# Kernel optimization log

Measured on AMD Instinct MI355X. Metric: run time of the kernel, lower is better.

The kernel has to match this reference:

```python
import jax, jax.numpy as jnp
import numpy as np

NUM_EXPERTS = 64
TOP_K = 6
ALPHA = 1e-3
HIDDEN = 128


def setup_inputs() -> dict:
    key = jax.random.key(0)
    k1, k2 = jax.random.split(key)
    hidden_states = jax.random.normal(k1, (64, 4096, HIDDEN), dtype=jnp.float32)
    # kaiming_uniform_(a=sqrt(5)) on weight of shape (64, 128): bound = 1/sqrt(fan_in)
    bound = 1.0 / np.sqrt(HIDDEN)
    W = jax.random.uniform(k2, (NUM_EXPERTS, HIDDEN), dtype=jnp.float32, minval=-bound, maxval=bound)
    return {"hidden_states": hidden_states, "W": W}


def reference(hidden_states, W):
    b, s, h = hidden_states.shape
    x = hidden_states.reshape(-1, h)                      # (N, h)
    logits = x @ W.T                                      # (N, 64)
    scores = jax.nn.softmax(logits, axis=-1)
    topk_weight, topk_idx = jax.lax.top_k(scores, TOP_K)  # (N, 6)
    # norm_topk_prob=True
    topk_weight = topk_weight / (topk_weight.sum(-1, keepdims=True) + 1e-20)
    # aux loss (training path, seq_aux=False): ce = one_hot(topk_idx).mean(0)
    counts = jnp.zeros(NUM_EXPERTS, dtype=scores.dtype).at[topk_idx.ravel()].add(1.0)
    ce = counts / jnp.asarray(topk_idx.size, scores.dtype)
    Pi = scores.mean(0)
    fi = ce * NUM_EXPERTS
    aux_loss = (Pi * fi).sum() * ALPHA
    return topk_idx, topk_weight, aux_loss
```

## Files before the change

### kernel.cpp

```cpp
#include <hip/hip_runtime.h>
#include <cfloat>

#define NTOK (64 * 4096)
#define HID  128
#define NE   64
#define TK   6
#define BLK  256
#define GRID (NTOK / BLK)

__global__ __launch_bounds__(BLK, 4)
void gate_kernel(const float* __restrict__ X,
                 const float* __restrict__ W,
                 float* __restrict__ oidx,
                 float* __restrict__ ow,
                 float* __restrict__ Pi_g,
                 unsigned int* __restrict__ cnt_g)
{
    __shared__ float        Wt[HID][NE];
    __shared__ float        Pi_s[NE];
    __shared__ unsigned int cnt_s[NE];

    const int tid  = threadIdx.x;
    const int lane = tid & 63;

    if (tid < NE) { Pi_s[tid] = 0.0f; cnt_s[tid] = 0u; }

    {
        const float4* W4 = (const float4*)W;
#pragma unroll
        for (int i = 0; i < 8; ++i) {
            const int flat = tid + i * BLK;
            const float4 v = W4[flat];
            const int e   = flat >> 5;
            const int k0  = (flat & 31) << 2;
            const int col = (e + ((flat & 15) << 2)) & 63;
            Wt[k0+0][col] = v.x; Wt[k0+1][col] = v.y;
            Wt[k0+2][col] = v.z; Wt[k0+3][col] = v.w;
        }
    }
    __syncthreads();

    const int token = blockIdx.x * BLK + tid;
    const float4* xrow = (const float4*)(X + (size_t)token * HID);

    float acc[NE];
#pragma unroll
    for (int e = 0; e < NE; ++e) acc[e] = 0.0f;

#pragma unroll 1
    for (int c = 0; c < 8; ++c) {
        float x[16];
#pragma unroll
        for (int j = 0; j < 4; ++j) {
            const float4 v = xrow[c*4 + j];
            x[4*j+0] = v.x; x[4*j+1] = v.y; x[4*j+2] = v.z; x[4*j+3] = v.w;
        }
#pragma unroll
        for (int kk = 0; kk < 16; ++kk) {
            const int row  = c*16 + kk;
            const int rot4 = (row >> 2) & 15;
            const float4* wrow = (const float4*)&Wt[row][0];
#pragma unroll
            for (int q = 0; q < 16; ++q) {
                const float4 w = wrow[(q + rot4) & 15];
                acc[4*q+0] = fmaf(x[kk], w.x, acc[4*q+0]);
                acc[4*q+1] = fmaf(x[kk], w.y, acc[4*q+1]);
                acc[4*q+2] = fmaf(x[kk], w.z, acc[4*q+2]);
                acc[4*q+3] = fmaf(x[kk], w.w, acc[4*q+3]);
            }
        }
    }

    float tv[TK];
    int   ti[TK];
#pragma unroll
    for (int q = 0; q < TK; ++q) { tv[q] = -FLT_MAX; ti[q] = 0; }

#pragma unroll
    for (int e = 0; e < NE; ++e) {
        float m = acc[e];
        int   mi = e;
#pragma unroll
        for (int q = 0; q < TK; ++q) {
            const bool  c  = m > tv[q];
            const float nt = c ? m     : tv[q];
            const float nm = c ? tv[q] : m;
            const int   ni = c ? mi    : ti[q];
            const int   nj = c ? ti[q] : mi;
            tv[q] = nt; m = nm; ti[q] = ni; mi = nj;
        }
    }

    const float mx = tv[0];
    float ex[TK];
    float s = 0.0f;
#pragma unroll
    for (int q = 0; q < TK; ++q) { ex[q] = __expf(tv[q] - mx); s += ex[q]; }
    const float rs = 1.0f / (s + 1e-20f);

    {
        const size_t gt = (size_t)token * TK;
        float2* ip = (float2*)(oidx + gt);
        float2* wp = (float2*)(ow + gt);
        ip[0] = make_float2((float)ti[0], (float)ti[1]);
        ip[1] = make_float2((float)ti[2], (float)ti[3]);
        ip[2] = make_float2((float)ti[4], (float)ti[5]);
        wp[0] = make_float2(ex[0]*rs, ex[1]*rs);
        wp[1] = make_float2(ex[2]*rs, ex[3]*rs);
        wp[2] = make_float2(ex[4]*rs, ex[5]*rs);
    }

#pragma unroll
    for (int q = 0; q < TK; ++q) atomicAdd(&cnt_s[ti[q]], 1u);

    float Z = 0.0f;
#pragma unroll
    for (int e = 0; e < NE; ++e) { acc[e] = __expf(acc[e] - mx); Z += acc[e]; }
    const float rz = 1.0f / Z;
#pragma unroll
    for (int e = 0; e < NE; ++e) acc[e] *= rz;

#pragma unroll
    for (int s = 32; s >= 1; s >>= 1) {
        const bool up = (lane & s) != 0;
#pragma unroll
        for (int i = 0; i < s; ++i) {
            const float lo = acc[i], hi = acc[i + s];
            const float send = up ? lo : hi;
            const float recv = __shfl_xor(send, s);
            acc[i] = (up ? hi : lo) + recv;
        }
    }
    atomicAdd(&Pi_s[lane], acc[0]);

    __syncthreads();
    if (tid < NE) {
        atomicAdd(&Pi_g[tid], Pi_s[tid]);
        atomicAdd(&cnt_g[tid], cnt_s[tid]);
    }
}

__global__ void aux_kernel(const float* __restrict__ Pi_g,
                           const unsigned int* __restrict__ cnt_g,
                           float* __restrict__ out_aux)
{
    const int e = threadIdx.x;
    const float Pi = Pi_g[e] * (1.0f / (float)NTOK);
    const float ce = (float)cnt_g[e] * (1.0f / (float)(NTOK * TK));
    float v = Pi * ce * (float)NE;
#pragma unroll
    for (int off = 32; off > 0; off >>= 1) v += __shfl_down(v, off);
    if (e == 0) out_aux[0] = v * 1.0e-3f;
}

extern "C" void kernel_launch(void* const* d_in, const int* in_sizes, int n_in,
                              void* d_out, int out_size, void* d_ws, size_t ws_size,
                              hipStream_t stream) {
    const float* X = (const float*)d_in[0];
    const float* W = (const float*)d_in[1];

    float* out  = (float*)d_out;
    float* oidx = out;
    float* ow   = out + (size_t)NTOK * TK;
    float* aux  = out + (size_t)NTOK * TK * 2;

    float*        Pi_g  = (float*)d_ws;
    unsigned int* cnt_g = (unsigned int*)((char*)d_ws + 256);

    hipMemsetAsync(d_ws, 0, 512, stream);
    gate_kernel<<<GRID, BLK, 0, stream>>>(X, W, oidx, ow, Pi_g, cnt_g);
    aux_kernel<<<1, 64, 0, stream>>>(Pi_g, cnt_g, aux);
}
```

Before: 258.0 us.

## Register-tile gate GEMM as 4 tokens x 8 experts per thread with staged X chunks

```diff
diff --git a/kernel.cpp b/kernel.cpp
--- a/kernel.cpp
+++ b/kernel.cpp
@@ -6,9 +6,14 @@
 #define NE   64
 #define TK   6
 #define BLK  256
-#define GRID (NTOK / BLK)
-
-__global__ __launch_bounds__(BLK, 4)
+#define TPB  128
+#define GRID (NTOK / TPB)
+#define WST  68
+#define XOFF (HID * WST)
+#define KC   16
+#define NCH  (HID / KC)
+
+__global__ __launch_bounds__(BLK, 3)
 void gate_kernel(const float* __restrict__ X,
                  const float* __restrict__ W,
                  float* __restrict__ oidx,
@@ -16,12 +21,18 @@
                  float* __restrict__ Pi_g,
                  unsigned int* __restrict__ cnt_g)
 {
-    __shared__ float        Wt[HID][NE];
+    __shared__ float smem[XOFF + TPB * KC];
     __shared__ float        Pi_s[NE];
     __shared__ unsigned int cnt_s[NE];
 
     const int tid  = threadIdx.x;
     const int lane = tid & 63;
+    const int wv   = tid >> 6;
+    const int tg   = lane >> 3;
+    const int eg   = lane & 7;
+    const int sw   = tg & 3;
+    const int tokL0 = wv * 32 + tg * 4;
+    const int gtok0 = blockIdx.x * TPB;
 
     if (tid < NE) { Pi_s[tid] = 0.0f; cnt_s[tid] = 0u; }
 
@@ -31,75 +42,107 @@
         for (int i = 0; i < 8; ++i) {
             const int flat = tid + i * BLK;
             const float4 v = W4[flat];
-            const int e   = flat >> 5;
-            const int k0  = (flat & 31) << 2;
-            const int col = (e + ((flat & 15) << 2)) & 63;
-            Wt[k0+0][col] = v.x; Wt[k0+1][col] = v.y;
-            Wt[k0+2][col] = v.z; Wt[k0+3][col] = v.w;
-        }
-    }
-    __syncthreads();
-
-    const int token = blockIdx.x * BLK + tid;
-    const float4* xrow = (const float4*)(X + (size_t)token * HID);
-
-    float acc[NE];
-#pragma unroll
-    for (int e = 0; e < NE; ++e) acc[e] = 0.0f;
+            const int e = flat >> 5, k4 = flat & 31;
+            smem[(4*k4+0)*WST + e] = v.x;
+            smem[(4*k4+1)*WST + e] = v.y;
+            smem[(4*k4+2)*WST + e] = v.z;
+            smem[(4*k4+3)*WST + e] = v.w;
+        }
+    }
+
+    float acc[4][8];
+#pragma unroll
+    for (int t = 0; t < 4; ++t)
+#pragma unroll
+        for (int j = 0; j < 8; ++j) acc[t][j] = 0.0f;
+
+    const float4* X4 = (const float4*)X;
 
 #pragma unroll 1
-    for (int c = 0; c < 8; ++c) {
-        float x[16];
-#pragma unroll
-        for (int j = 0; j < 4; ++j) {
-            const float4 v = xrow[c*4 + j];
-            x[4*j+0] = v.x; x[4*j+1] = v.y; x[4*j+2] = v.z; x[4*j+3] = v.w;
-        }
-#pragma unroll
-        for (int kk = 0; kk < 16; ++kk) {
-            const int row  = c*16 + kk;
-            const int rot4 = (row >> 2) & 15;
-            const float4* wrow = (const float4*)&Wt[row][0];
-#pragma unroll
-            for (int q = 0; q < 16; ++q) {
-                const float4 w = wrow[(q + rot4) & 15];
-                acc[4*q+0] = fmaf(x[kk], w.x, acc[4*q+0]);
-                acc[4*q+1] = fmaf(x[kk], w.y, acc[4*q+1]);
-                acc[4*q+2] = fmaf(x[kk], w.z, acc[4*q+2]);
-                acc[4*q+3] = fmaf(x[kk], w.w, acc[4*q+3]);
+    for (int c = 0; c < NCH; ++c) {
+        __syncthreads();
+#pragma unroll
+        for (int i = 0; i < 2; ++i) {
+            const int flat  = tid + i * BLK;
+            const int token = flat >> 2, g = flat & 3;
+            const float4 v = X4[(size_t)(gtok0 + token) * (HID/4) + c*4 + g];
+            *(float4*)&smem[XOFF + token*KC + ((g ^ ((token>>2)&3)) << 2)] = v;
+        }
+        __syncthreads();
+
+        const float* wb = smem + c * KC * WST;
+#pragma unroll
+        for (int g = 0; g < 4; ++g) {
+            float xs[4][4];
+#pragma unroll
+            for (int t = 0; t < 4; ++t) {
+                const float4 v = *(const float4*)&smem[XOFF + (tokL0+t)*KC + ((g ^ sw) << 2)];
+                xs[t][0] = v.x; xs[t][1] = v.y; xs[t][2] = v.z; xs[t][3] = v.w;
             }
-        }
-    }
-
-    float tv[TK];
-    int   ti[TK];
-#pragma unroll
-    for (int q = 0; q < TK; ++q) { tv[q] = -FLT_MAX; ti[q] = 0; }
-
-#pragma unroll
-    for (int e = 0; e < NE; ++e) {
-        float m = acc[e];
-        int   mi = e;
-#pragma unroll
-        for (int q = 0; q < TK; ++q) {
-            const bool  c  = m > tv[q];
-            const float nt = c ? m     : tv[q];
-            const float nm = c ? tv[q] : m;
-            const int   ni = c ? mi    : ti[q];
-            const int   nj = c ? ti[q] : mi;
-            tv[q] = nt; m = nm; ti[q] = ni; mi = nj;
-        }
-    }
-
-    const float mx = tv[0];
-    float ex[TK];
-    float s = 0.0f;
-#pragma unroll
-    for (int q = 0; q < TK; ++q) { ex[q] = __expf(tv[q] - mx); s += ex[q]; }
-    const float rs = 1.0f / (s + 1e-20f);
-
-    {
-        const size_t gt = (size_t)token * TK;
+#pragma unroll
+            for (int j = 0; j < 4; ++j) {
+                const float4 w0 = *(const float4*)&wb[(g*4+j)*WST + 8*eg];
+                const float4 w1 = *(const float4*)&wb[(g*4+j)*WST + 8*eg + 4];
+#pragma unroll
+                for (int t = 0; t < 4; ++t) {
+                    const float xv = xs[t][j];
+                    acc[t][0] = fmaf(xv, w0.x, acc[t][0]);
+                    acc[t][1] = fmaf(xv, w0.y, acc[t][1]);
+                    acc[t][2] = fmaf(xv, w0.z, acc[t][2]);
+                    acc[t][3] = fmaf(xv, w0.w, acc[t][3]);
+                    acc[t][4] = fmaf(xv, w1.x, acc[t][4]);
+                    acc[t][5] = fmaf(xv, w1.y, acc[t][5]);
+                    acc[t][6] = fmaf(xv, w1.z, acc[t][6]);
+                    acc[t][7] = fmaf(xv, w1.w, acc[t][7]);
+                }
+            }
+        }
+    }
+
+    __syncthreads();
+
+#pragma unroll
+    for (int t = 0; t < 4; ++t) {
+        *(float4*)&smem[(tokL0+t)*WST + 8*eg    ] =
+            make_float4(acc[t][0], acc[t][1], acc[t][2], acc[t][3]);
+        *(float4*)&smem[(tokL0+t)*WST + 8*eg + 4] =
+            make_float4(acc[t][4], acc[t][5], acc[t][6], acc[t][7]);
+    }
+    __syncthreads();
+
+    if (tid < TPB) {
+        const int t = tid;
+        const float* Lrow = &smem[t * WST];
+        float tv[TK]; int ti[TK];
+#pragma unroll
+        for (int q = 0; q < TK; ++q) { tv[q] = -FLT_MAX; ti[q] = 0; }
+
+#pragma unroll 4
+        for (int e4 = 0; e4 < 16; ++e4) {
+            const float4 v4 = *(const float4*)&Lrow[e4 * 4];
+            const float vv[4] = {v4.x, v4.y, v4.z, v4.w};
+#pragma unroll
+            for (int u = 0; u < 4; ++u) {
+                float m = vv[u]; int mi = e4*4 + u;
+#pragma unroll
+                for (int q = 0; q < TK; ++q) {
+                    const bool  cx = m > tv[q];
+                    const float nt = cx ? m     : tv[q];
+                    const float nm = cx ? tv[q] : m;
+                    const int   ni = cx ? mi    : ti[q];
+                    const int   nj = cx ? ti[q] : mi;
+                    tv[q] = nt; m = nm; ti[q] = ni; mi = nj;
+                }
+            }
+        }
+
+        const float mx = tv[0];
+        float ex[TK]; float s = 0.0f;
+#pragma unroll
+        for (int q = 0; q < TK; ++q) { ex[q] = __expf(tv[q] - mx); s += ex[q]; }
+        const float rs = 1.0f / (s + 1e-20f);
+
+        const size_t gt = (size_t)(gtok0 + t) * TK;
         float2* ip = (float2*)(oidx + gt);
         float2* wp = (float2*)(ow + gt);
         ip[0] = make_float2((float)ti[0], (float)ti[1]);
@@ -108,30 +151,35 @@
         wp[0] = make_float2(ex[0]*rs, ex[1]*rs);
         wp[1] = make_float2(ex[2]*rs, ex[3]*rs);
         wp[2] = make_float2(ex[4]*rs, ex[5]*rs);
-    }
-
-#pragma unroll
-    for (int q = 0; q < TK; ++q) atomicAdd(&cnt_s[ti[q]], 1u);
-
-    float Z = 0.0f;
-#pragma unroll
-    for (int e = 0; e < NE; ++e) { acc[e] = __expf(acc[e] - mx); Z += acc[e]; }
-    const float rz = 1.0f / Z;
-#pragma unroll
-    for (int e = 0; e < NE; ++e) acc[e] *= rz;
-
-#pragma unroll
-    for (int s = 32; s >= 1; s >>= 1) {
-        const bool up = (lane & s) != 0;
-#pragma unroll
-        for (int i = 0; i < s; ++i) {
-            const float lo = acc[i], hi = acc[i + s];
-            const float send = up ? lo : hi;
-            const float recv = __shfl_xor(send, s);
-            acc[i] = (up ? hi : lo) + recv;
-        }
-    }
-    atomicAdd(&Pi_s[lane], acc[0]);
+
+#pragma unroll
+        for (int q = 0; q < TK; ++q) atomicAdd(&cnt_s[ti[q]], 1u);
+
+        float Z = 0.0f;
+#pragma unroll 4
+        for (int e4 = 0; e4 < 16; ++e4) {
+            const float4 v4 = *(const float4*)&Lrow[e4 * 4];
+            Z += __expf(v4.x - mx); Z += __expf(v4.y - mx);
+            Z += __expf(v4.z - mx); Z += __expf(v4.w - mx);
+        }
+        smem[XOFF + 2*t]     = mx;
+        smem[XOFF + 2*t + 1] = 1.0f / Z;
+    }
+    __syncthreads();
+
+    float pi[8];
+#pragma unroll
+    for (int j = 0; j < 8; ++j) pi[j] = 0.0f;
+#pragma unroll
+    for (int t = 0; t < 4; ++t) {
+        const float mxt = smem[XOFF + 2*(tokL0+t)];
+        const float rzt = smem[XOFF + 2*(tokL0+t) + 1];
+#pragma unroll
+        for (int j = 0; j < 8; ++j)
+            pi[j] += __expf(acc[t][j] - mxt) * rzt;
+    }
+#pragma unroll
+    for (int j = 0; j < 8; ++j) atomicAdd(&Pi_s[8*eg + j], pi[j]);
 
     __syncthreads();
     if (tid < NE) {
```

Measured after the change: 270.7 us. 4.9% more time.

## Split experts across waves with multi-token register tiles and LDS-staged logits

Applied to the files above, without the earlier changes.

```diff
diff --git a/kernel.cpp b/kernel.cpp
--- a/kernel.cpp
+++ b/kernel.cpp
@@ -6,9 +6,11 @@
 #define NE   64
 #define TK   6
 #define BLK  256
-#define GRID (NTOK / BLK)
-
-__global__ __launch_bounds__(BLK, 4)
+#define TPB  256
+#define GRID (NTOK / TPB)
+#define LST  67
+
+__global__ __launch_bounds__(BLK, 2)
 void gate_kernel(const float* __restrict__ X,
                  const float* __restrict__ W,
                  float* __restrict__ oidx,
@@ -16,14 +18,17 @@
                  float* __restrict__ Pi_g,
                  unsigned int* __restrict__ cnt_g)
 {
-    __shared__ float        Wt[HID][NE];
+    __shared__ float        smem[TPB * LST];
+    __shared__ float        mz[2 * TPB];
     __shared__ float        Pi_s[NE];
     __shared__ unsigned int cnt_s[NE];
 
     const int tid  = threadIdx.x;
     const int lane = tid & 63;
-
-    if (tid < NE) { Pi_s[tid] = 0.0f; cnt_s[tid] = 0u; }
+    const int wv   = __builtin_amdgcn_readfirstlane(tid >> 6);
+    const int eb   = wv * 16;
+
+    if (tid < NE) cnt_s[tid] = 0u;
 
     {
         const float4* W4 = (const float4*)W;
@@ -32,74 +37,114 @@
             const int flat = tid + i * BLK;
             const float4 v = W4[flat];
             const int e   = flat >> 5;
-            const int k0  = (flat & 31) << 2;
-            const int col = (e + ((flat & 15) << 2)) & 63;
-            Wt[k0+0][col] = v.x; Wt[k0+1][col] = v.y;
-            Wt[k0+2][col] = v.z; Wt[k0+3][col] = v.w;
-        }
-    }
-    __syncthreads();
-
-    const int token = blockIdx.x * BLK + tid;
-    const float4* xrow = (const float4*)(X + (size_t)token * HID);
-
-    float acc[NE];
-#pragma unroll
-    for (int e = 0; e < NE; ++e) acc[e] = 0.0f;
-
-#pragma unroll 1
-    for (int c = 0; c < 8; ++c) {
-        float x[16];
-#pragma unroll
-        for (int j = 0; j < 4; ++j) {
-            const float4 v = xrow[c*4 + j];
-            x[4*j+0] = v.x; x[4*j+1] = v.y; x[4*j+2] = v.z; x[4*j+3] = v.w;
-        }
-#pragma unroll
-        for (int kk = 0; kk < 16; ++kk) {
-            const int row  = c*16 + kk;
-            const int rot4 = (row >> 2) & 15;
-            const float4* wrow = (const float4*)&Wt[row][0];
-#pragma unroll
-            for (int q = 0; q < 16; ++q) {
-                const float4 w = wrow[(q + rot4) & 15];
-                acc[4*q+0] = fmaf(x[kk], w.x, acc[4*q+0]);
-                acc[4*q+1] = fmaf(x[kk], w.y, acc[4*q+1]);
-                acc[4*q+2] = fmaf(x[kk], w.z, acc[4*q+2]);
-                acc[4*q+3] = fmaf(x[kk], w.w, acc[4*q+3]);
+            const int c   = flat & 31;
+            const int col = (e + ((c & 15) << 2)) & 63;
+            float* p = &smem[c * 256 + col];
+            p[0]   = v.x;
+            p[64]  = v.y;
+            p[128] = v.z;
+            p[192] = v.w;
+        }
+    }
+    __syncthreads();
+
+    const int gtok0 = blockIdx.x * TPB;
+    const float4* xr0 = (const float4*)(X + (size_t)(gtok0 + lane      ) * HID);
+    const float4* xr1 = (const float4*)(X + (size_t)(gtok0 + lane +  64) * HID);
+    const float4* xr2 = (const float4*)(X + (size_t)(gtok0 + lane + 128) * HID);
+    const float4* xr3 = (const float4*)(X + (size_t)(gtok0 + lane + 192) * HID);
+
+    float acc[4][16];
+#pragma unroll
+    for (int g = 0; g < 4; ++g)
+#pragma unroll
+        for (int j = 0; j < 16; ++j) acc[g][j] = 0.0f;
+
+#pragma unroll 2
+    for (int c = 0; c < 32; ++c) {
+        float xs[4][4];
+        {
+            const float4 v0 = xr0[c], v1 = xr1[c], v2 = xr2[c], v3 = xr3[c];
+            xs[0][0]=v0.x; xs[0][1]=v0.y; xs[0][2]=v0.z; xs[0][3]=v0.w;
+            xs[1][0]=v1.x; xs[1][1]=v1.y; xs[1][2]=v1.z; xs[1][3]=v1.w;
+            xs[2][0]=v2.x; xs[2][1]=v2.y; xs[2][2]=v2.z; xs[2][3]=v2.w;
+            xs[3][0]=v3.x; xs[3][1]=v3.y; xs[3][2]=v3.z; xs[3][3]=v3.w;
+        }
+        const int rr = (c & 15) << 2;
+        const int c0 = (eb +  0 + rr) & 63;
+        const int c1 = (eb +  4 + rr) & 63;
+        const int c2 = (eb +  8 + rr) & 63;
+        const int c3 = (eb + 12 + rr) & 63;
+        const float* rowb = &smem[c * 256];
+#pragma unroll
+        for (int d = 0; d < 4; ++d) {
+            const float* row = rowb + d * 64;
+            const float4 w0 = *(const float4*)&row[c0];
+            const float4 w1 = *(const float4*)&row[c1];
+            const float4 w2 = *(const float4*)&row[c2];
+            const float4 w3 = *(const float4*)&row[c3];
+#pragma unroll
+            for (int g = 0; g < 4; ++g) {
+                const float xv = xs[g][d];
+                acc[g][ 0] = fmaf(xv, w0.x, acc[g][ 0]);
+                acc[g][ 1] = fmaf(xv, w0.y, acc[g][ 1]);
+                acc[g][ 2] = fmaf(xv, w0.z, acc[g][ 2]);
+                acc[g][ 3] = fmaf(xv, w0.w, acc[g][ 3]);
+                acc[g][ 4] = fmaf(xv, w1.x, acc[g][ 4]);
+                acc[g][ 5] = fmaf(xv, w1.y, acc[g][ 5]);
+                acc[g][ 6] = fmaf(xv, w1.z, acc[g][ 6]);
+                acc[g][ 7] = fmaf(xv, w1.w, acc[g][ 7]);
+                acc[g][ 8] = fmaf(xv, w2.x, acc[g][ 8]);
+                acc[g][ 9] = fmaf(xv, w2.y, acc[g][ 9]);
+                acc[g][10] = fmaf(xv, w2.z, acc[g][10]);
+                acc[g][11] = fmaf(xv, w2.w, acc[g][11]);
+                acc[g][12] = fmaf(xv, w3.x, acc[g][12]);
+                acc[g][13] = fmaf(xv, w3.y, acc[g][13]);
+                acc[g][14] = fmaf(xv, w3.z, acc[g][14]);
+                acc[g][15] = fmaf(xv, w3.w, acc[g][15]);
             }
         }
     }
 
-    float tv[TK];
-    int   ti[TK];
-#pragma unroll
-    for (int q = 0; q < TK; ++q) { tv[q] = -FLT_MAX; ti[q] = 0; }
-
-#pragma unroll
-    for (int e = 0; e < NE; ++e) {
-        float m = acc[e];
-        int   mi = e;
-#pragma unroll
-        for (int q = 0; q < TK; ++q) {
-            const bool  c  = m > tv[q];
-            const float nt = c ? m     : tv[q];
-            const float nm = c ? tv[q] : m;
-            const int   ni = c ? mi    : ti[q];
-            const int   nj = c ? ti[q] : mi;
-            tv[q] = nt; m = nm; ti[q] = ni; mi = nj;
-        }
-    }
-
-    const float mx = tv[0];
-    float ex[TK];
-    float s = 0.0f;
-#pragma unroll
-    for (int q = 0; q < TK; ++q) { ex[q] = __expf(tv[q] - mx); s += ex[q]; }
-    const float rs = 1.0f / (s + 1e-20f);
+    __syncthreads();
+
+#pragma unroll
+    for (int g = 0; g < 4; ++g) {
+        float* p = &smem[(lane + 64 * g) * LST + eb];
+#pragma unroll
+        for (int j = 0; j < 16; ++j) p[j] = acc[g][j];
+    }
+    __syncthreads();
 
     {
-        const size_t gt = (size_t)token * TK;
+        const int t = tid;
+        const float* Lrow = &smem[t * LST];
+        float tv[TK]; int ti[TK];
+#pragma unroll
+        for (int q = 0; q < TK; ++q) { tv[q] = -FLT_MAX; ti[q] = 0; }
+
+#pragma unroll 8
+        for (int e = 0; e < NE; ++e) {
+            float m = Lrow[e];
+            int   mi = e;
+#pragma unroll
+            for (int q = 0; q < TK; ++q) {
+                const bool  cx = m > tv[q];
+                const float nt = cx ? m     : tv[q];
+                const float nm = cx ? tv[q] : m;
+                const int   ni = cx ? mi    : ti[q];
+                const int   nj = cx ? ti[q] : mi;
+                tv[q] = nt; m = nm; ti[q] = ni; mi = nj;
+            }
+        }
+
+        const float mx = tv[0];
+        float ex[TK]; float s = 0.0f;
+#pragma unroll
+        for (int q = 0; q < TK; ++q) { ex[q] = __expf(tv[q] - mx); s += ex[q]; }
+        const float rs = 1.0f / (s + 1e-20f);
+
+        const size_t gt = (size_t)(gtok0 + t) * TK;
         float2* ip = (float2*)(oidx + gt);
         float2* wp = (float2*)(ow + gt);
         ip[0] = make_float2((float)ti[0], (float)ti[1]);
@@ -108,32 +153,41 @@
         wp[0] = make_float2(ex[0]*rs, ex[1]*rs);
         wp[1] = make_float2(ex[2]*rs, ex[3]*rs);
         wp[2] = make_float2(ex[4]*rs, ex[5]*rs);
-    }
-
-#pragma unroll
-    for (int q = 0; q < TK; ++q) atomicAdd(&cnt_s[ti[q]], 1u);
-
-    float Z = 0.0f;
-#pragma unroll
-    for (int e = 0; e < NE; ++e) { acc[e] = __expf(acc[e] - mx); Z += acc[e]; }
-    const float rz = 1.0f / Z;
-#pragma unroll
-    for (int e = 0; e < NE; ++e) acc[e] *= rz;
-
-#pragma unroll
-    for (int s = 32; s >= 1; s >>= 1) {
-        const bool up = (lane & s) != 0;
-#pragma unroll
-        for (int i = 0; i < s; ++i) {
-            const float lo = acc[i], hi = acc[i + s];
-            const float send = up ? lo : hi;
-            const float recv = __shfl_xor(send, s);
-            acc[i] = (up ? hi : lo) + recv;
-        }
-    }
-    atomicAdd(&Pi_s[lane], acc[0]);
-
-    __syncthreads();
+
+#pragma unroll
+        for (int q = 0; q < TK; ++q) atomicAdd(&cnt_s[ti[q]], 1u);
+
+        float Z = 0.0f;
+#pragma unroll 8
+        for (int e = 0; e < NE; ++e) Z += __expf(Lrow[e] - mx);
+        mz[2*t]     = mx;
+        mz[2*t + 1] = 1.0f / Z;
+    }
+    __syncthreads();
+
+    {
+        float pi[16];
+#pragma unroll
+        for (int j = 0; j < 16; ++j) pi[j] = 0.0f;
+#pragma unroll
+        for (int g = 0; g < 4; ++g) {
+            const int t = lane + 64 * g;
+            const float mxt = mz[2*t];
+            const float rzt = mz[2*t + 1];
+            const float* p = &smem[t * LST + eb];
+#pragma unroll
+            for (int j = 0; j < 16; ++j)
+                pi[j] += __expf(p[j] - mxt) * rzt;
+        }
+#pragma unroll
+        for (int s = 1; s <= 32; s <<= 1) {
+#pragma unroll
+            for (int j = 0; j < 16; ++j) pi[j] += __shfl_xor(pi[j], s);
+        }
+        if (lane < 16) Pi_s[eb + lane] = pi[lane];
+    }
+    __syncthreads();
+
     if (tid < NE) {
         atomicAdd(&Pi_g[tid], Pi_s[tid]);
         atomicAdd(&cnt_g[tid], cnt_s[tid]);
```

Measured after the change: 257.8 us. No clear change (-0.1%).
